# Optimization experiments

Hardware: AMD Instinct MI355X
Metric: run time of the kernel (lower is better)

Reference implementation:

```python
import jax, jax.numpy as jnp
import numpy as np

K_SIZE = 7  # matches init_kwargs k_size
EPS = 1e-7


def setup_inputs() -> dict:
    key = jax.random.key(0)
    x = jax.random.normal(key, (4, 64, 128, 128), dtype=jnp.float32)
    return {"x": x}


def reference(x):
    K = K_SIZE
    P = K // 2
    B, C, H, W = x.shape
    # zero-pad spatially, same as F.unfold(padding=K//2)
    xp = jnp.pad(x, ((0, 0), (0, 0), (P, P), (P, P)))
    # gather k*k shifted views -> (B, C, K*K, H, W); fixed small loop over window offsets
    patches = jnp.stack(
        [xp[:, :, i:i + H, j:j + W] for i in range(K) for j in range(K)], axis=2
    )
    # dot product of center pixel with each neighbor over channels -> (B, K*K, H, W)
    sim = jnp.sum(x[:, :, None, :, :] * patches, axis=1)
    norm_center = jnp.sqrt(jnp.sum(x * x, axis=1))[:, None]          # (B,1,H,W)
    norm_patches = jnp.sqrt(jnp.sum(patches * patches, axis=1))       # (B,K*K,H,W)
    sim = sim / (norm_center * norm_patches + EPS)
    sim = jax.nn.softmax(sim, axis=1)  # softmax over the K*K window dim
    return sim.reshape(B, K * K, H * W)
```

## Files before the change

### kernel.cpp

```cpp
#include <hip/hip_runtime.h>
#include <math.h>

#define KK 49
#define H 128
#define W 128
#define C 64
#define NB 4
#define EPS 1e-7f
#define PLANE (H * W)

#define TW 32
#define TH 2
#define HW2 38
#define HH2 8
#define NPOS (HW2 * HH2)
#define NP2 (2 * NPOS)
#define CADDR (3 * HW2 + 3)


template<int Q>
__device__ __forceinline__ void compute_q(const float4* __restrict__ basep,
                                          float (&acc)[13]) {
    constexpr int NK = (Q == 3) ? 13 : 12;
    const float4 c0 = basep[CADDR];
    const float4 c1 = basep[NPOS + CADDR];
#pragma unroll
    for (int l = 0; l < NK; ++l) {
        const int k = Q * 12 + l;
        const int off = (k / 7) * HW2 + (k % 7);
        const float4 n0 = basep[off];
        const float4 n1 = basep[NPOS + off];
        acc[l] += c0.x * n0.x; acc[l] += c0.y * n0.y;
        acc[l] += c0.z * n0.z; acc[l] += c0.w * n0.w;
        acc[l] += c1.x * n1.x; acc[l] += c1.y * n1.y;
        acc[l] += c1.z * n1.z; acc[l] += c1.w * n1.w;
    }
}

template<int Q>
__device__ __forceinline__ void sim_and_max(const float* __restrict__ snb,
                                            float (&acc)[13], float& m) {
    constexpr int NK = (Q == 3) ? 13 : 12;
    const float nc = snb[CADDR];
#pragma unroll
    for (int l = 0; l < NK; ++l) {
        const int k = Q * 12 + l;
        const int off = (k / 7) * HW2 + (k % 7);
        const float nn = snb[off];
        const float sv = __fdividef(acc[l], nc * nn + EPS);
        acc[l] = sv;
        m = fmaxf(m, sv);
    }
}

template<int Q>
__device__ __forceinline__ void exp_and_sum(float (&acc)[13], float m, float& sum) {
    constexpr int NK = (Q == 3) ? 13 : 12;
#pragma unroll
    for (int l = 0; l < NK; ++l) {
        const float e = __expf(acc[l] - m);
        acc[l] = e;
        sum += e;
    }
}

template<int Q>
__device__ __forceinline__ void store_q(float* __restrict__ op,
                                        const float (&acc)[13], float inv) {
    constexpr int NK = (Q == 3) ? 13 : 12;
#pragma unroll
    for (int l = 0; l < NK; ++l)
        op[(size_t)l << 14] = acc[l] * inv;
}

#define DISPATCH_Q(stmt)                                      \
    do {                                                      \
        if (s2 == 0)      { constexpr int Q = 0; stmt; }      \
        else if (s2 == 1) { constexpr int Q = 1; stmt; }      \
        else if (s2 == 2) { constexpr int Q = 2; stmt; }      \
        else              { constexpr int Q = 3; stmt; }      \
    } while (0)

__global__ __launch_bounds__(256, 2) void rsa_kernel(const float* __restrict__ x,
                                                     float* __restrict__ out) {
    __shared__ float4 sx[2][NP2];
    __shared__ float  sn2[NP2];
    __shared__ float  snf[NPOS];
    __shared__ float  comb[4][TW * TH];

    const int tid = threadIdx.x;
    const int w   = tid & 31;
    const int r   = (tid >> 5) & 1;
    const int s2  = tid >> 6;
    const int w0  = blockIdx.x * TW;
    const int h0  = blockIdx.y * TH;
    const int b   = blockIdx.z;
    const float* __restrict__ xb = x + (size_t)b * C * PLANE;

    const int roww = r * HW2 + w;
    const float4* const base4[2] = { &sx[0][0] + roww, &sx[1][0] + roww };

    int goff[3], pos[3], hh[3];
    bool act[3], inb[3];
#pragma unroll
    for (int j = 0; j < 3; ++j) {
        int i = tid + j * 256;
        act[j] = (i < NP2);
        int ii = act[j] ? i : 0;
        int h  = (ii >= NPOS) ? 1 : 0;
        int p  = ii - h * NPOS;
        int rr = p / HW2, cc = p - rr * HW2;
        int gh = h0 - 3 + rr, gw = w0 - 3 + cc;
        inb[j]  = (gh >= 0) && (gh < H) && (gw >= 0) && (gw < W);
        goff[j] = gh * W + gw;
        pos[j]  = ii;
        hh[j]   = h;
    }

    float4 pf[3];
    float  np[3] = {0.f, 0.f, 0.f};

    auto load_pass = [&](int t) {
#pragma unroll
        for (int j = 0; j < 3; ++j) {
            float4 v = make_float4(0.f, 0.f, 0.f, 0.f);
            if (act[j] && inb[j]) {
                const float* p = xb + (size_t)(t * 8 + hh[j] * 4) * PLANE + goff[j];
                v.x = p[0];
                v.y = p[PLANE];
                v.z = p[2 * PLANE];
                v.w = p[3 * PLANE];
            }
            pf[j] = v;
        }
    };

    auto write_pass = [&](int buf) {
#pragma unroll
        for (int j = 0; j < 3; ++j) {
            if (act[j]) {
                sx[buf][pos[j]] = pf[j];
                float4 v = pf[j];
                np[j] += v.x * v.x + v.y * v.y + v.z * v.z + v.w * v.w;
            }
        }
    };

    float acc[13];
#pragma unroll
    for (int l = 0; l < 13; ++l) acc[l] = 0.f;

    load_pass(0);
    write_pass(0);
    __syncthreads();
#pragma unroll 2
    for (int t = 0; t < 8; ++t) {
        const int buf = t & 1;
        if (t < 7) load_pass(t + 1);
        DISPATCH_Q(compute_q<Q>(base4[buf], acc));
        if (t < 7) write_pass(buf ^ 1);
        __syncthreads();
    }

#pragma unroll
    for (int j = 0; j < 3; ++j)
        if (act[j]) sn2[pos[j]] = np[j];
    __syncthreads();
    for (int i = tid; i < NPOS; i += 256) snf[i] = sqrtf(sn2[i] + sn2[i + NPOS]);
    __syncthreads();

    const float* snb = &snf[0] + roww;
    float m = -1e30f;
    DISPATCH_Q(sim_and_max<Q>(snb, acc, m));

    const int pxi = r * TW + w;
    comb[s2][pxi] = m;
    __syncthreads();
    m = fmaxf(fmaxf(comb[0][pxi], comb[1][pxi]), fmaxf(comb[2][pxi], comb[3][pxi]));
    __syncthreads();

    float sum = 0.f;
    DISPATCH_Q(exp_and_sum<Q>(acc, m, sum));
    comb[s2][pxi] = sum;
    __syncthreads();
    sum = (comb[0][pxi] + comb[1][pxi]) + (comb[2][pxi] + comb[3][pxi]);
    const float inv = __fdividef(1.f, sum);

    float* op = out + (((size_t)b * KK + s2 * 12) << 14) + ((h0 + r) << 7) + (w0 + w);
    DISPATCH_Q(store_q<Q>(op, acc, inv));
}

extern "C" void kernel_launch(void* const* d_in, const int* in_sizes, int n_in,
                              void* d_out, int out_size, void* d_ws, size_t ws_size,
                              hipStream_t stream) {
    const float* x = (const float*)d_in[0];
    float* out = (float*)d_out;

    dim3 block(256, 1, 1);
    dim3 grid(W / TW, H / TH, NB);
    rsa_kernel<<<grid, block, 0, stream>>>(x, out);
}
```

Before: 82.92 us.

## Stage channels as packed fp16 and use fdot2 for dot products and norms

Input channels are converted to packed half2 on load, using round-toward-zero conversion. Each shared-memory uint4 now holds 8 channels instead of 4, which halves the number of pipeline stages and the LDS traffic per channel. The similarity dot products and squared norms are computed with v_dot2 fp16 instructions that accumulate in fp32. This lowers precision: fp16 rounding of the inputs perturbs the cosine similarities, and large values could overflow.

```diff
diff --git a/kernel.cpp b/kernel.cpp
--- a/kernel.cpp
+++ b/kernel.cpp
@@ -18,22 +18,36 @@
 #define CADDR (3 * HW2 + 3)
 
 
-template<int Q>
-__device__ __forceinline__ void compute_q(const float4* __restrict__ basep,
+typedef _Float16 h2_t __attribute__((ext_vector_type(2)));
+
+__device__ __forceinline__ float fdot2(unsigned int a, unsigned int b, float c) {
+    return __builtin_amdgcn_fdot2(__builtin_bit_cast(h2_t, a),
+                                  __builtin_bit_cast(h2_t, b), c, false);
+}
+__device__ __forceinline__ unsigned int packh2(float a, float b) {
+    return __builtin_bit_cast(unsigned int, __builtin_amdgcn_cvt_pkrtz(a, b));
+}
+
+template<int Q>
+__device__ __forceinline__ void compute_q(const uint4* __restrict__ bp,
                                           float (&acc)[13]) {
     constexpr int NK = (Q == 3) ? 13 : 12;
-    const float4 c0 = basep[CADDR];
-    const float4 c1 = basep[NPOS + CADDR];
+    const uint4 c0 = bp[CADDR];
+    const uint4 c1 = bp[NPOS + CADDR];
 #pragma unroll
     for (int l = 0; l < NK; ++l) {
         const int k = Q * 12 + l;
         const int off = (k / 7) * HW2 + (k % 7);
-        const float4 n0 = basep[off];
-        const float4 n1 = basep[NPOS + off];
-        acc[l] += c0.x * n0.x; acc[l] += c0.y * n0.y;
-        acc[l] += c0.z * n0.z; acc[l] += c0.w * n0.w;
-        acc[l] += c1.x * n1.x; acc[l] += c1.y * n1.y;
-        acc[l] += c1.z * n1.z; acc[l] += c1.w * n1.w;
+        const uint4 n0 = bp[off];
+        const uint4 n1 = bp[NPOS + off];
+        acc[l] = fdot2(c0.x, n0.x, acc[l]);
+        acc[l] = fdot2(c0.y, n0.y, acc[l]);
+        acc[l] = fdot2(c0.z, n0.z, acc[l]);
+        acc[l] = fdot2(c0.w, n0.w, acc[l]);
+        acc[l] = fdot2(c1.x, n1.x, acc[l]);
+        acc[l] = fdot2(c1.y, n1.y, acc[l]);
+        acc[l] = fdot2(c1.z, n1.z, acc[l]);
+        acc[l] = fdot2(c1.w, n1.w, acc[l]);
     }
 }
 
@@ -83,10 +97,10 @@
 
 __global__ __launch_bounds__(256, 2) void rsa_kernel(const float* __restrict__ x,
                                                      float* __restrict__ out) {
-    __shared__ float4 sx[2][NP2];
-    __shared__ float  sn2[NP2];
-    __shared__ float  snf[NPOS];
-    __shared__ float  comb[4][TW * TH];
+    __shared__ uint4 sx[2][NP2];
+    __shared__ float sn2[NP2];
+    __shared__ float snf[NPOS];
+    __shared__ float comb[4][TW * TH];
 
     const int tid = threadIdx.x;
     const int w   = tid & 31;
@@ -98,7 +112,7 @@
     const float* __restrict__ xb = x + (size_t)b * C * PLANE;
 
     const int roww = r * HW2 + w;
-    const float4* const base4[2] = { &sx[0][0] + roww, &sx[1][0] + roww };
+    const uint4* const base4[2] = { &sx[0][0] + roww, &sx[1][0] + roww };
 
     int goff[3], pos[3], hh[3];
     bool act[3], inb[3];
@@ -107,31 +121,39 @@
         int i = tid + j * 256;
         act[j] = (i < NP2);
         int ii = act[j] ? i : 0;
-        int h  = (ii >= NPOS) ? 1 : 0;
-        int p  = ii - h * NPOS;
+        int g  = (ii >= NPOS) ? 1 : 0;
+        int p  = ii - g * NPOS;
         int rr = p / HW2, cc = p - rr * HW2;
         int gh = h0 - 3 + rr, gw = w0 - 3 + cc;
         inb[j]  = (gh >= 0) && (gh < H) && (gw >= 0) && (gw < W);
         goff[j] = gh * W + gw;
         pos[j]  = ii;
-        hh[j]   = h;
-    }
-
-    float4 pf[3];
-    float  np[3] = {0.f, 0.f, 0.f};
+        hh[j]   = g;
+    }
+
+    uint4 pu[3];
+    float np[3] = {0.f, 0.f, 0.f};
 
     auto load_pass = [&](int t) {
 #pragma unroll
         for (int j = 0; j < 3; ++j) {
-            float4 v = make_float4(0.f, 0.f, 0.f, 0.f);
+            uint4 u = make_uint4(0u, 0u, 0u, 0u);
             if (act[j] && inb[j]) {
-                const float* p = xb + (size_t)(t * 8 + hh[j] * 4) * PLANE + goff[j];
-                v.x = p[0];
-                v.y = p[PLANE];
-                v.z = p[2 * PLANE];
-                v.w = p[3 * PLANE];
+                const float* p = xb + (size_t)(t * 16 + hh[j] * 8) * PLANE + goff[j];
+                const float f0 = p[0];
+                const float f1 = p[PLANE];
+                const float f2 = p[2 * PLANE];
+                const float f3 = p[3 * PLANE];
+                const float f4 = p[4 * PLANE];
+                const float f5 = p[5 * PLANE];
+                const float f6 = p[6 * PLANE];
+                const float f7 = p[7 * PLANE];
+                u.x = packh2(f0, f1);
+                u.y = packh2(f2, f3);
+                u.z = packh2(f4, f5);
+                u.w = packh2(f6, f7);
             }
-            pf[j] = v;
+            pu[j] = u;
         }
     };
 
@@ -139,9 +161,11 @@
 #pragma unroll
         for (int j = 0; j < 3; ++j) {
             if (act[j]) {
-                sx[buf][pos[j]] = pf[j];
-                float4 v = pf[j];
-                np[j] += v.x * v.x + v.y * v.y + v.z * v.z + v.w * v.w;
+                sx[buf][pos[j]] = pu[j];
+                np[j] = fdot2(pu[j].x, pu[j].x, np[j]);
+                np[j] = fdot2(pu[j].y, pu[j].y, np[j]);
+                np[j] = fdot2(pu[j].z, pu[j].z, np[j]);
+                np[j] = fdot2(pu[j].w, pu[j].w, np[j]);
             }
         }
     };
@@ -153,12 +177,12 @@
     load_pass(0);
     write_pass(0);
     __syncthreads();
-#pragma unroll 2
-    for (int t = 0; t < 8; ++t) {
+#pragma unroll
+    for (int t = 0; t < 4; ++t) {
         const int buf = t & 1;
-        if (t < 7) load_pass(t + 1);
+        if (t < 3) load_pass(t + 1);
         DISPATCH_Q(compute_q<Q>(base4[buf], acc));
-        if (t < 7) write_pass(buf ^ 1);
+        if (t < 3) write_pass(buf ^ 1);
         __syncthreads();
     }
 
```

Measured after the change: 81.33 us. No clear change (-1.9%).
